# Kernel tuning notes

Measured on AMD Instinct MI355X. Metric: run time of the kernel, lower is better.

The kernel has to match this reference:

```python
import jax, jax.numpy as jnp
import numpy as np

B, N, D_MODEL = 4, 4096, 1024
HEADS, DIM_HEAD = 8, 64
INNER = HEADS * DIM_HEAD  # 512
NB_FEAT = int(DIM_HEAD * np.log(DIM_HEAD))  # 266, performer default
D_FF = 4 * D_MODEL
KERNEL_EPS = 1e-4
LN_EPS = 1e-5


def setup_inputs() -> dict:
    key = jax.random.key(0)
    ks = jax.random.split(key, 12)
    w = lambda i, shape: jax.random.normal(ks[i], shape, jnp.float32) * 0.02
    z = lambda *shape: jnp.zeros(shape, jnp.float32)
    o = lambda *shape: jnp.ones(shape, jnp.float32)
    return dict(
        x=jax.random.normal(ks[0], (B, N, D_MODEL), jnp.float32),
        proj_w=w(1, (D_MODEL, D_MODEL)), proj_b=z(D_MODEL),
        ln1_g=o(D_MODEL), ln1_b=z(D_MODEL),
        wq=w(2, (D_MODEL, INNER)), bq=z(INNER),
        wk=w(3, (D_MODEL, INNER)), bk=z(INNER),
        wv=w(4, (D_MODEL, INNER)), bv=z(INNER),
        wo=w(5, (INNER, D_MODEL)), bo=z(D_MODEL),
        proj_mat=jax.random.normal(ks[6], (NB_FEAT, DIM_HEAD), jnp.float32),
        ln2_g=o(D_MODEL), ln2_b=z(D_MODEL),
        w1=w(7, (D_MODEL, D_FF)), b1=z(D_FF),
        w2=w(8, (D_FF, D_MODEL)), b2=z(D_MODEL),
    )


def _layer_norm(x, g, b):
    mu = x.mean(-1, keepdims=True)
    var = ((x - mu) ** 2).mean(-1, keepdims=True)
    return (x - mu) * jax.lax.rsqrt(var + LN_EPS) * g + b


def _softmax_kernel(data, proj_mat, is_query):
    # data: [b,h,n,d], proj_mat: [m,d] -> features [b,h,n,m]
    dn = DIM_HEAD ** -0.25            # data_normalizer
    ratio = NB_FEAT ** -0.5
    dd = jnp.einsum('bhnd,md->bhnm', data * dn, proj_mat)
    diag = (data ** 2).sum(-1, keepdims=True) * (0.5 * dn * dn)
    if is_query:
        mx = dd.max(-1, keepdims=True)
    else:
        mx = dd.max(axis=(-1, -2), keepdims=True)
    return ratio * (jnp.exp(dd - diag - mx) + KERNEL_EPS)


def _favor_attention(q, k, v, proj_mat):
    # non-causal FAVOR+ linear attention; q,k,v: [b,h,n,d]
    qp = _softmax_kernel(q, proj_mat, True)    # [b,h,n,m]
    kp = _softmax_kernel(k, proj_mat, False)   # [b,h,n,m]
    k_sum = kp.sum(-2)                         # [b,h,m]
    d_inv = 1.0 / jnp.einsum('bhnm,bhm->bhn', qp, k_sum)
    ctx = jnp.einsum('bhnm,bhnd->bhmd', kp, v)
    return jnp.einsum('bhmd,bhnm,bhn->bhnd', ctx, qp, d_inv)


def _performer(x, ln1_g, ln1_b, wq, bq, wk, bk, wv, bv, wo, bo, proj_mat,
               ln2_g, ln2_b, w1, b1, w2, b2):
    # pre-norm self-attention block
    h = _layer_norm(x, ln1_g, ln1_b)
    split = lambda t: t.reshape(B, N, HEADS, DIM_HEAD).transpose(0, 2, 1, 3)
    q = split(h @ wq + bq)
    k = split(h @ wk + bk)
    v = split(h @ wv + bv)
    attn = _favor_attention(q, k, v, proj_mat)
    attn = attn.transpose(0, 2, 1, 3).reshape(B, N, INNER)
    x = x + attn @ wo + bo
    # pre-norm feed-forward block
    h = _layer_norm(x, ln2_g, ln2_b)
    x = x + jax.nn.gelu(h @ w1 + b1, approximate=False) @ w2 + b2
    return x


def reference(x, proj_w, proj_b, ln1_g, ln1_b, wq, bq, wk, bk, wv, bv,
              wo, bo, proj_mat, ln2_g, ln2_b, w1, b1, w2, b2):
    u = x @ proj_w + proj_b                    # dense gate branch
    v = _performer(x, ln1_g, ln1_b, wq, bq, wk, bk, wv, bv, wo, bo,
                   proj_mat, ln2_g, ln2_b, w1, b1, w2, b2)
    return u * v
```

## Files before the change

### kernel.cpp

```cpp
#include <hip/hip_runtime.h>
#include <math.h>

typedef unsigned short bf16_t;
using bf16x8 = __attribute__((ext_vector_type(8))) short;
using f32x4  = __attribute__((ext_vector_type(4))) float;

#define DEVFN static __device__ __forceinline__

DEVFN float b2f(bf16_t u){ unsigned v=((unsigned)u)<<16; float f; __builtin_memcpy(&f,&v,4); return f; }
DEVFN bf16_t f2b(float f){ unsigned u; __builtin_memcpy(&u,&f,4); u += 0x7fffu + ((u>>16)&1u); return (bf16_t)(u>>16); }
DEVFN unsigned encf(float f){ unsigned u=__float_as_uint(f); return (u&0x80000000u)? ~u : (u|0x80000000u); }
DEVFN float decf(unsigned e){ return __uint_as_float((e&0x80000000u)? (e^0x80000000u) : ~e); }

DEVFN float erf_fast(float x){
  float ax = fabsf(x);
  float t = __builtin_amdgcn_rcpf(1.0f + 0.3275911f*ax);
  float y = t*(0.254829592f + t*(-0.284496736f + t*(1.421413741f
          + t*(-1.453152027f + t*1.061405429f))));
  float r = 1.0f - y*__expf(-ax*ax);
  return copysignf(r, x);
}

constexpr float DN_SCALE = 0.35355339059327373f;
constexpr float RATIO    = 0.06131393394849658f;
constexpr float KEPS     = 1e-4f;
#define MPAD 288

#define GLOAD_LDS16(g, l) __builtin_amdgcn_global_load_lds( \
    (__attribute__((address_space(1))) void*)(g), \
    (__attribute__((address_space(3))) void*)(l), 16, 0, 0)

#define MFMA16(a,b,c) __builtin_amdgcn_mfma_f32_16x16x32_bf16(a,b,c,0,0,0)

__global__ __launch_bounds__(256)
void wt_cast(const float* __restrict__ W, bf16_t* __restrict__ Wt, int K, int N)
{
  __shared__ alignas(16) float ts[32][33];
  int t = threadIdx.x;
  int r = t>>3, c4 = (t&7)*4;
  int k0 = blockIdx.x*32, n0 = blockIdx.y*32;
  float4 v = *(const float4*)(W + (size_t)(k0+r)*N + n0 + c4);
  ts[r][c4+0]=v.x; ts[r][c4+1]=v.y; ts[r][c4+2]=v.z; ts[r][c4+3]=v.w;
  __syncthreads();
  ushort4 o;
  o.x = f2b(ts[c4+0][r]); o.y = f2b(ts[c4+1][r]);
  o.z = f2b(ts[c4+2][r]); o.w = f2b(ts[c4+3][r]);
  *(ushort4*)(Wt + (size_t)(n0+r)*K + k0 + c4) = o;
}

__global__ __launch_bounds__(256)
void concat_bias(const float* __restrict__ bq, const float* __restrict__ bk,
                 const float* __restrict__ bv, float* __restrict__ dst)
{
  int t = blockIdx.x*256 + threadIdx.x;
  if (t < 512) dst[t] = bq[t];
  else if (t < 1024) dst[t] = bk[t-512];
  else dst[t] = bv[t-1024];
}

__global__ void mx_init(unsigned* m){ if (threadIdx.x < 32) m[threadIdx.x] = 0u; }

__global__ void zero_out(float* o, long n){
  long i = (long)blockIdx.x*256 + threadIdx.x;
  if (i < n) o[i] = 0.f;
}

__global__ __launch_bounds__(256)
void pm_cast(const float* __restrict__ pm, bf16_t* __restrict__ pmb)
{
  int idx = blockIdx.x*256 + threadIdx.x;
  int r = idx>>6, c = idx&63;
  pmb[idx] = (r < 266) ? f2b(pm[r*64+c]*DN_SCALE) : (bf16_t)0;
}

__global__ __launch_bounds__(256)
void diag_kernel(const bf16_t* __restrict__ qkv, float* __restrict__ diagq,
                 float* __restrict__ diagk)
{
  int bh = blockIdx.y, b = bh>>3, h = bh&7;
  int n = blockIdx.x*256 + threadIdx.x;
  long trow = (long)b*4096 + n;
  const bf16_t* qp_ = qkv + trow*1536 + h*64;
  const bf16_t* kp_ = qkv + trow*1536 + 512 + h*64;
  float sq = 0.f, sk = 0.f;
  #pragma unroll
  for (int i=0;i<8;i++){
    uint4 cq = ((const uint4*)qp_)[i];
    uint4 ck = ((const uint4*)kp_)[i];
    unsigned w[4] = {cq.x,cq.y,cq.z,cq.w};
    unsigned v[4] = {ck.x,ck.y,ck.z,ck.w};
    #pragma unroll
    for (int j=0;j<4;j++){
      float a0=b2f((bf16_t)(w[j]&0xffff)), a1=b2f((bf16_t)(w[j]>>16));
      float b0=b2f((bf16_t)(v[j]&0xffff)), b1=b2f((bf16_t)(v[j]>>16));
      sq += a0*a0 + a1*a1; sk += b0*b0 + b1*b1;
    }
  }
  float sc = 0.5f*DN_SCALE*DN_SCALE;
  diagq[(long)bh*4096 + n] = sq*sc;
  diagk[(long)bh*4096 + n] = sk*sc;
}

__global__ __launch_bounds__(256)
void vt_trans(const bf16_t* __restrict__ qkv, bf16_t* __restrict__ vT)
{
  __shared__ ushort ts[32][36];
  int by = blockIdx.y;
  int bh = by>>1, dt = by&1, b = bh>>3, h = bh&7;
  int n0 = blockIdx.x*32;
  int t = threadIdx.x, r = t>>3, c4 = (t&7)*4;
  ushort4 v = *(const ushort4*)(qkv + ((size_t)b*4096 + n0 + r)*1536 + 1024 + h*64 + dt*32 + c4);
  ts[r][c4+0]=v.x; ts[r][c4+1]=v.y; ts[r][c4+2]=v.z; ts[r][c4+3]=v.w;
  __syncthreads();
  ushort4 o;
  o.x = ts[c4+0][r]; o.y = ts[c4+1][r]; o.z = ts[c4+2][r]; o.w = ts[c4+3][r];
  *(ushort4*)(vT + ((size_t)bh*64 + dt*32 + r)*4096 + n0 + c4) = o;
}

__global__ __launch_bounds__(256)
void ln_kernel(const float* __restrict__ x, const float* __restrict__ g,
               const float* __restrict__ b, bf16_t* __restrict__ out)
{
  long row = blockIdx.x; int t = threadIdx.x;
  float4 v = ((const float4*)x)[row*256 + t];
  float s = v.x+v.y+v.z+v.w;
  #pragma unroll
  for (int o=32;o>0;o>>=1) s += __shfl_xor(s, o);
  __shared__ float r1[4], r2[4];
  if ((t&63)==0) r1[t>>6] = s;
  __syncthreads();
  float mu = (r1[0]+r1[1]+r1[2]+r1[3]) * (1.f/1024.f);
  float dx = v.x-mu, dy = v.y-mu, dz = v.z-mu, dw = v.w-mu;
  float ss = dx*dx+dy*dy+dz*dz+dw*dw;
  #pragma unroll
  for (int o=32;o>0;o>>=1) ss += __shfl_xor(ss, o);
  if ((t&63)==0) r2[t>>6] = ss;
  __syncthreads();
  float var = (r2[0]+r2[1]+r2[2]+r2[3]) * (1.f/1024.f);
  float rs = rsqrtf(var + 1e-5f);
  float4 gg = ((const float4*)g)[t], bb = ((const float4*)b)[t];
  ushort4 o4;
  o4.x = f2b(dx*rs*gg.x+bb.x); o4.y = f2b(dy*rs*gg.y+bb.y);
  o4.z = f2b(dz*rs*gg.z+bb.z); o4.w = f2b(dw*rs*gg.w+bb.w);
  ((ushort4*)out)[row*256+t] = o4;
}

__global__ __launch_bounds__(256)
void cast_f32_bf16(const float* __restrict__ in, bf16_t* __restrict__ out)
{
  long i = (long)blockIdx.x*256 + threadIdx.x;
  float4 v = ((const float4*)in)[i];
  ushort4 o;
  o.x = f2b(v.x); o.y = f2b(v.y); o.z = f2b(v.z); o.w = f2b(v.w);
  ((ushort4*)out)[i] = o;
}

template<int RES, int GELU, int GATEF, int OBF>
__global__ __launch_bounds__(256)
void gemm_bt(const bf16_t* __restrict__ A, int lda,
             const bf16_t* __restrict__ Bt, int ldb,
             const float* __restrict__ bias,
             const float* res,
             const float* gatef,
             void* Cout, int N, int K)
{
  __shared__ alignas(16) bf16_t As[2][128*32];
  __shared__ alignas(16) bf16_t Bs[2][128*32];
  const int tid = threadIdx.x;
  const int wid = tid>>6, lane = tid&63;
  const int l15 = lane&15, l4 = lane>>4;
  const int wm = wid>>1, wn = wid&1;

  const int NX = gridDim.x;
  const int nwg = NX * gridDim.y;
  const int lid = blockIdx.y*NX + blockIdx.x;
  const int qc = nwg>>3;
  const int wgid = (lid&7)*qc + (lid>>3);
  const int stripe = wgid / (16*NX);
  const int rem    = wgid % (16*NX);
  const long m0 = (long)(stripe*16 + (rem & 15))*128;
  const long n0 = (long)(rem >> 4)*128;

  f32x4 acc[4][4];
  #pragma unroll
  for (int i=0;i<4;i++)
    #pragma unroll
    for (int j=0;j<4;j++) acc[i][j] = f32x4{0.f,0.f,0.f,0.f};

  const bf16_t* ga = A  + (size_t)(m0 + (tid>>2))*lda + (tid&3)*8;
  const bf16_t* gb = Bt + (size_t)(n0 + (tid>>2))*ldb + (tid&3)*8;

  auto STAGE = [&](int buf){
    GLOAD_LDS16(ga,                   &As[buf][wid*512]);
    GLOAD_LDS16(ga + (size_t)64*lda,  &As[buf][2048 + wid*512]);
    GLOAD_LDS16(gb,                   &Bs[buf][wid*512]);
    GLOAD_LDS16(gb + (size_t)64*ldb,  &Bs[buf][2048 + wid*512]);
    ga += 32; gb += 32;
  };

  const int nt = K >> 5;
  STAGE(0);
  __syncthreads();
  int cur = 0;
  for (int t = 0; t < nt; ++t){
    if (t+1 < nt) STAGE(cur^1);
    bf16x8 af[4], bfr[4];
    #pragma unroll
    for (int i=0;i<4;i++){
      af[i]  = *(const bf16x8*)(&As[cur][(wm*64 + i*16 + l15)*32 + l4*8]);
      bfr[i] = *(const bf16x8*)(&Bs[cur][(wn*64 + i*16 + l15)*32 + l4*8]);
    }
    #pragma unroll
    for (int i=0;i<4;i++)
      #pragma unroll
      for (int j=0;j<4;j++)
        acc[i][j] = MFMA16(af[i], bfr[j], acc[i][j]);
    __syncthreads();
    cur ^= 1;
  }

  #pragma unroll
  for (int i=0;i<4;i++){
    #pragma unroll
    for (int j=0;j<4;j++){
      #pragma unroll
      for (int r=0;r<4;r++){
        long row = m0 + wm*64 + i*16 + l4*4 + r;
        long col = n0 + wn*64 + j*16 + l15;
        float v = acc[i][j][r] + bias[col];
        if constexpr (RES)   v += res[row*(long)N + col];
        if constexpr (GELU)  v = 0.5f*v*(1.0f + erf_fast(v*0.70710678118654752f));
        if constexpr (GATEF) v *= gatef[row*(long)N + col];
        if constexpr (OBF)  ((bf16_t*)Cout)[row*(long)N + col] = f2b(v);
        else                ((float* )Cout)[row*(long)N + col] = v;
      }
    }
  }
}


__global__ __launch_bounds__(256,2)
void favor_kmax2(const bf16_t* __restrict__ qkv, const bf16_t* __restrict__ pmb,
                 unsigned* __restrict__ mxk)
{
  int bh = blockIdx.y, b = bh>>3, h = bh&7;
  int t = threadIdx.x, wid = t>>6, lane = t&63;
  int l15 = lane&15, l4 = lane>>4;
  int n0 = blockIdx.x*64, row0 = wid*16;
  f32x4 acc[18];
  #pragma unroll
  for (int c=0;c<18;c++) acc[c] = f32x4{0.f,0.f,0.f,0.f};
  const bf16_t* abase = qkv + ((size_t)(b*4096) + n0 + row0 + l15)*1536 + 512 + h*64;
  #pragma unroll
  for (int kh=0;kh<2;kh++){
    bf16x8 a = *(const bf16x8*)(abase + kh*32 + l4*8);
    #pragma unroll
    for (int ct=0;ct<18;ct++){
      bf16x8 bb = *(const bf16x8*)(pmb + (ct*16+l15)*64 + kh*32 + l4*8);
      acc[ct] = MFMA16(a, bb, acc[ct]);
    }
  }
  float mx = -3e38f;
  #pragma unroll
  for (int ct=0;ct<18;ct++){
    if (ct*16 + l15 < 266){
      #pragma unroll
      for (int r=0;r<4;r++) mx = fmaxf(mx, acc[ct][r]);
    }
  }
  #pragma unroll
  for (int o=32;o>0;o>>=1) mx = fmaxf(mx, __shfl_xor(mx, o));
  __shared__ float red[4];
  if (lane==0) red[wid] = mx;
  __syncthreads();
  if (t==0){
    float m2 = fmaxf(fmaxf(red[0],red[1]),fmaxf(red[2],red[3]));
    atomicMax(mxk + bh, encf(m2));
  }
}

__global__ __launch_bounds__(256,2)
void favor_kp(const bf16_t* __restrict__ qkv, const bf16_t* __restrict__ pmb,
              const unsigned* __restrict__ mxk, const float* __restrict__ diagk,
              bf16_t* __restrict__ kp, int bh0)
{
  int bhl = blockIdx.y, bh = bh0 + bhl, b = bh>>3, h = bh&7;
  int t = threadIdx.x, wid = t>>6, lane = t&63;
  int l15 = lane&15, l4 = lane>>4;
  int n0 = blockIdx.x*64, row0 = wid*16;
  f32x4 acc[18];
  #pragma unroll
  for (int c=0;c<18;c++) acc[c] = f32x4{0.f,0.f,0.f,0.f};
  const bf16_t* abase = qkv + ((size_t)(b*4096) + n0 + row0 + l15)*1536 + 512 + h*64;
  #pragma unroll
  for (int kh=0;kh<2;kh++){
    bf16x8 a = *(const bf16x8*)(abase + kh*32 + l4*8);
    #pragma unroll
    for (int ct=0;ct<18;ct++){
      bf16x8 bb = *(const bf16x8*)(pmb + (ct*16+l15)*64 + kh*32 + l4*8);
      acc[ct] = MFMA16(a, bb, acc[ct]);
    }
  }
  float MX = decf(mxk[bh]);
  float dg[4];
  #pragma unroll
  for (int r=0;r<4;r++) dg[r] = diagk[(size_t)bh*4096 + n0 + row0 + l4*4 + r];
  #pragma unroll
  for (int ct=0;ct<18;ct++){
    int col = ct*16 + l15;
    #pragma unroll
    for (int r=0;r<4;r++){
      float v = (col < 266) ? RATIO*(__expf(acc[ct][r] - dg[r] - MX) + KEPS) : 0.f;
      kp[((size_t)bhl*4096 + n0 + row0 + l4*4 + r)*MPAD + col] = f2b(v);
    }
  }
}

__global__ __launch_bounds__(256)
void trans_kp(const bf16_t* __restrict__ kp, bf16_t* __restrict__ kpT)
{
  __shared__ ushort ts[32][36];
  int bhl = blockIdx.z;
  int n0 = blockIdx.x*32, m0 = blockIdx.y*32;
  int t = threadIdx.x, r = t>>3, c4 = (t&7)*4;
  ushort4 v = *(const ushort4*)(kp + ((size_t)bhl*4096 + n0 + r)*MPAD + m0 + c4);
  ts[r][c4+0]=v.x; ts[r][c4+1]=v.y; ts[r][c4+2]=v.z; ts[r][c4+3]=v.w;
  __syncthreads();
  ushort4 o;
  o.x = ts[c4+0][r]; o.y = ts[c4+1][r]; o.z = ts[c4+2][r]; o.w = ts[c4+3][r];
  *(ushort4*)(kpT + ((size_t)bhl*MPAD + m0 + r)*4096 + n0 + c4) = o;
}

__global__ __launch_bounds__(256)
void ksum_kernel(const bf16_t* __restrict__ kpT, float* __restrict__ ksumf, int bh0)
{
  int t = threadIdx.x, wid = t>>6, lane = t&63;
  int rr = blockIdx.x*4 + wid;
  int bhl = rr/272, m = rr%272;
  const bf16_t* row = kpT + ((size_t)bhl*MPAD + m)*4096;
  float s = 0.f;
  #pragma unroll
  for (int j=0;j<8;j++){
    bf16x8 v = *(const bf16x8*)(row + j*512 + lane*8);
    #pragma unroll
    for (int e=0;e<8;e++) s += b2f((bf16_t)v[e]);
  }
  #pragma unroll
  for (int o=32;o>0;o>>=1) s += __shfl_xor(s, o);
  if (lane==0) ksumf[(size_t)(bh0+bhl)*MPAD + m] = s;
}

__global__ __launch_bounds__(256,2)
void ctx_gemm(const bf16_t* __restrict__ kpT, const bf16_t* __restrict__ vT,
              float* __restrict__ ctxP, int bh0)
{
  int m0 = blockIdx.x*16, ks = blockIdx.y, bhl = blockIdx.z, bh = bh0 + bhl;
  int t = threadIdx.x, wid = t>>6, lane = t&63;
  int l15 = lane&15, l4 = lane>>4;
  f32x4 acc[4];
  #pragma unroll
  for (int c=0;c<4;c++) acc[c] = f32x4{0.f,0.f,0.f,0.f};
  const bf16_t* Abase = kpT + ((size_t)bhl*MPAD + m0 + l15)*4096;
  const bf16_t* Bbase = vT + ((size_t)bh*64)*4096;
  const int kb = ks*1024 + wid*256;
  for (int k = kb; k < kb + 256; k += 32){
    bf16x8 a = *(const bf16x8*)(Abase + k + l4*8);
    #pragma unroll
    for (int ct=0;ct<4;ct++){
      bf16x8 bb = *(const bf16x8*)(Bbase + (size_t)(ct*16+l15)*4096 + k + l4*8);
      acc[ct] = MFMA16(a, bb, acc[ct]);
    }
  }
  __shared__ float red[4][4][16][16];
  #pragma unroll
  for (int ct=0;ct<4;ct++)
    #pragma unroll
    for (int r=0;r<4;r++) red[wid][ct][l4*4+r][l15] = acc[ct][r];
  __syncthreads();
  #pragma unroll
  for (int i=0;i<4;i++){
    int e = i*256 + t;
    int ct = e>>8, row = (e>>4)&15, col = e&15;
    float s = ((red[0][ct][row][col] + red[1][ct][row][col])
             + (red[2][ct][row][col] + red[3][ct][row][col]));
    ctxP[(((size_t)bhl*4 + ks)*272 + m0 + row)*64 + ct*16 + col] = s;
  }
}

__global__ __launch_bounds__(256)
void ctx_reduce(const float* __restrict__ ctxP, bf16_t* __restrict__ ctxT, int bh0)
{
  int bhl = blockIdx.y, bh = bh0 + bhl;
  int idx = blockIdx.x*256 + threadIdx.x;
  int m = idx>>6, d = idx&63;
  float s = 0.f;
  #pragma unroll
  for (int ks=0;ks<4;ks++)
    s += ctxP[(((size_t)bhl*4 + ks)*272 + m)*64 + d];
  ctxT[((size_t)bh*64 + d)*MPAD + m] = f2b(s);
}

__global__ __launch_bounds__(256,2)
void favor_q(const bf16_t* __restrict__ qkv, const bf16_t* __restrict__ pmb,
             const float* __restrict__ diagq, const float* __restrict__ ksumf,
             const bf16_t* __restrict__ ctxT, bf16_t* __restrict__ attn)
{
  __shared__ alignas(16) ushort qpLds[64*296];
  __shared__ float ksLds[288];
  int bh = blockIdx.y, b = bh>>3, h = bh&7;
  int t = threadIdx.x, wid = t>>6, lane = t&63;
  int l15 = lane&15, l4 = lane>>4;
  int n0 = blockIdx.x*64, row0 = wid*16;
  ksLds[t] = ksumf[(size_t)bh*MPAD + t];
  if (t < 32) ksLds[256+t] = ksumf[(size_t)bh*MPAD + 256 + t];
  __syncthreads();

  f32x4 acc[18];
  #pragma unroll
  for (int c=0;c<18;c++) acc[c] = f32x4{0.f,0.f,0.f,0.f};
  const bf16_t* abase = qkv + ((size_t)(b*4096) + n0 + row0 + l15)*1536 + h*64;
  #pragma unroll
  for (int kh=0;kh<2;kh++){
    bf16x8 a = *(const bf16x8*)(abase + kh*32 + l4*8);
    #pragma unroll
    for (int ct=0;ct<18;ct++){
      bf16x8 bb = *(const bf16x8*)(pmb + (ct*16+l15)*64 + kh*32 + l4*8);
      acc[ct] = MFMA16(a, bb, acc[ct]);
    }
  }
  float mxr[4] = {-3e38f,-3e38f,-3e38f,-3e38f};
  #pragma unroll
  for (int ct=0;ct<18;ct++){
    if (ct*16 + l15 < 266){
      #pragma unroll
      for (int r=0;r<4;r++) mxr[r] = fmaxf(mxr[r], acc[ct][r]);
    }
  }
  #pragma unroll
  for (int r=0;r<4;r++){
    mxr[r] = fmaxf(mxr[r], __shfl_xor(mxr[r], 1));
    mxr[r] = fmaxf(mxr[r], __shfl_xor(mxr[r], 2));
    mxr[r] = fmaxf(mxr[r], __shfl_xor(mxr[r], 4));
    mxr[r] = fmaxf(mxr[r], __shfl_xor(mxr[r], 8));
  }
  float dg[4];
  #pragma unroll
  for (int r=0;r<4;r++) dg[r] = diagq[(size_t)bh*4096 + n0 + row0 + l4*4 + r];
  float den[4] = {0.f,0.f,0.f,0.f};
  #pragma unroll
  for (int ct=0;ct<18;ct++){
    int col = ct*16 + l15;
    float ks = ksLds[col];
    #pragma unroll
    for (int r=0;r<4;r++){
      float qpv = 0.f;
      if (col < 266){
        qpv = RATIO*(__expf(acc[ct][r] - dg[r] - mxr[r]) + KEPS);
        den[r] += qpv*ks;
      }
      qpLds[(row0 + l4*4 + r)*296 + col] = f2b(qpv);
    }
  }
  float dinv[4];
  #pragma unroll
  for (int r=0;r<4;r++){
    den[r] += __shfl_xor(den[r], 1);
    den[r] += __shfl_xor(den[r], 2);
    den[r] += __shfl_xor(den[r], 4);
    den[r] += __shfl_xor(den[r], 8);
    dinv[r] = 1.0f/den[r];
  }
  __syncthreads();

  f32x4 o2[4];
  #pragma unroll
  for (int c=0;c<4;c++) o2[c] = f32x4{0.f,0.f,0.f,0.f};
  const bf16_t* Bbase = ctxT + (size_t)bh*64*MPAD;
  #pragma unroll
  for (int kk=0;kk<9;kk++){
    int k0 = kk*32;
    bf16x8 a = *(const bf16x8*)&qpLds[(row0 + l15)*296 + k0 + l4*8];
    #pragma unroll
    for (int ct=0;ct<4;ct++){
      bf16x8 bb = *(const bf16x8*)(Bbase + (size_t)(ct*16+l15)*MPAD + k0 + l4*8);
      o2[ct] = MFMA16(a, bb, o2[ct]);
    }
  }
  #pragma unroll
  for (int ct=0;ct<4;ct++)
    #pragma unroll
    for (int r=0;r<4;r++)
      attn[((size_t)(b*4096) + n0 + row0 + l4*4 + r)*512 + h*64 + ct*16 + l15]
        = f2b(o2[ct][r] * dinv[r]);
}

extern "C" void kernel_launch(void* const* d_in, const int* in_sizes, int n_in,
                              void* d_out, int out_size, void* d_ws, size_t ws_size,
                              hipStream_t stream)
{
  (void)in_sizes; (void)n_in; (void)out_size;
  const float* x      = (const float*)d_in[0];
  const float* proj_w = (const float*)d_in[1];
  const float* proj_b = (const float*)d_in[2];
  const float* ln1_g  = (const float*)d_in[3];
  const float* ln1_b  = (const float*)d_in[4];
  const float* wq     = (const float*)d_in[5];
  const float* bq     = (const float*)d_in[6];
  const float* wk     = (const float*)d_in[7];
  const float* bk     = (const float*)d_in[8];
  const float* wv     = (const float*)d_in[9];
  const float* bv     = (const float*)d_in[10];
  const float* wo     = (const float*)d_in[11];
  const float* bo     = (const float*)d_in[12];
  const float* pm     = (const float*)d_in[13];
  const float* ln2_g  = (const float*)d_in[14];
  const float* ln2_b  = (const float*)d_in[15];
  const float* w1     = (const float*)d_in[16];
  const float* b1     = (const float*)d_in[17];
  const float* w2     = (const float*)d_in[18];
  const float* b2     = (const float*)d_in[19];
  float* out = (float*)d_out;
  const size_t MB = 1ull<<20;

  char* ws = (char*)d_ws;
  size_t off = 0;
  auto alloc = [&](size_t bytes)->void*{ void* p = ws + off; off += (bytes + 255) & ~(size_t)255; return p; };
  bf16_t* Wt_proj = (bf16_t*)alloc(2ul*1024*1024);
  bf16_t* Wt_qkv  = (bf16_t*)alloc(2ul*1536*1024);
  bf16_t* Wt_o    = (bf16_t*)alloc(2ul*1024*512);
  bf16_t* Wt_1    = (bf16_t*)alloc(2ul*4096*1024);
  bf16_t* Wt_2    = (bf16_t*)alloc(2ul*1024*4096);
  float*  bqkv    = (float*) alloc(4ul*1536);
  unsigned* mxk   = (unsigned*)alloc(4ul*32);
  bf16_t* pmb     = (bf16_t*)alloc(2ul*MPAD*64);
  float*  diagq   = (float*) alloc(4ul*32*4096);
  float*  diagk   = (float*) alloc(4ul*32*4096);
  float*  ksumf   = (float*) alloc(4ul*32*MPAD);
  bf16_t* ctxT    = (bf16_t*)alloc(2ul*32*64*MPAD);
  float*  ctxP    = (float*) alloc(4ul*8*4*272*64);
  char*   R       = (char*)  alloc(0);
  size_t R_avail = (ws_size > off) ? ws_size - off : 0;

  if (R_avail < 67*MB){ zero_out<<<dim3(65536), 256, 0, stream>>>(out, 16777216L); return; }
  int KG = (R_avail >= 87*MB) ? 8 : 4;
  int NC = (R_avail >= 84*MB) ? 2 : 4;

  bf16_t* qkv  = (bf16_t*)(R);
  bf16_t* h1c  = (bf16_t*)(R + 48*MB);
  bf16_t* kp   = (bf16_t*)(R + 48*MB);
  bf16_t* kpT  = (bf16_t*)(R + 48*MB + (size_t)KG*4096*MPAD*2 + 1*MB);
  bf16_t* attn = (bf16_t*)(R + 48*MB);
  long    CH   = 16384/NC;
  bf16_t* h2c  = (bf16_t*)(R);
  bf16_t* ff1c = (bf16_t*)(R + 16*MB);
  bf16_t* vT   = (bf16_t*)d_out;

  wt_cast<<<dim3(32,32), 256, 0, stream>>>(proj_w, Wt_proj, 1024, 1024);
  wt_cast<<<dim3(32,16), 256, 0, stream>>>(wq, Wt_qkv,              1024, 512);
  wt_cast<<<dim3(32,16), 256, 0, stream>>>(wk, Wt_qkv + 512*1024,   1024, 512);
  wt_cast<<<dim3(32,16), 256, 0, stream>>>(wv, Wt_qkv + 1024*1024,  1024, 512);
  wt_cast<<<dim3(16,32), 256, 0, stream>>>(wo, Wt_o, 512, 1024);
  wt_cast<<<dim3(32,128),256, 0, stream>>>(w1, Wt_1, 1024, 4096);
  wt_cast<<<dim3(128,32),256, 0, stream>>>(w2, Wt_2, 4096, 1024);
  concat_bias<<<dim3(6), 256, 0, stream>>>(bq, bk, bv, bqkv);
  pm_cast<<<dim3(72), 256, 0, stream>>>(pm, pmb);

  for (int c = 0; c < 2; c++){
    ln_kernel<<<dim3(8192), 256, 0, stream>>>(x + (size_t)c*8192*1024, ln1_g, ln1_b, h1c);
    gemm_bt<0,0,0,1><<<dim3(12,64), 256, 0, stream>>>(h1c, 1024, Wt_qkv, 1024,
        bqkv, nullptr, nullptr, qkv + (size_t)c*8192*1536, 1536, 1024);
  }

  diag_kernel<<<dim3(16,32), 256, 0, stream>>>(qkv, diagq, diagk);
  vt_trans<<<dim3(128,64), 256, 0, stream>>>(qkv, vT);
  mx_init<<<dim3(1), 64, 0, stream>>>(mxk);
  favor_kmax2<<<dim3(64,32), 256, 0, stream>>>(qkv, pmb, mxk);
  for (int g = 0; g < 32; g += KG){
    favor_kp<<<dim3(64,KG), 256, 0, stream>>>(qkv, pmb, mxk, diagk, kp, g);
    trans_kp<<<dim3(128,9,KG), 256, 0, stream>>>(kp, kpT);
    ksum_kernel<<<dim3(KG*68), 256, 0, stream>>>(kpT, ksumf, g);
    ctx_gemm<<<dim3(17,4,KG), 256, 0, stream>>>(kpT, vT, ctxP, g);
    ctx_reduce<<<dim3(68,KG), 256, 0, stream>>>(ctxP, ctxT, g);
  }
  favor_q<<<dim3(64,32), 256, 0, stream>>>(qkv, pmb, diagq, ksumf, ctxT, attn);

  gemm_bt<1,0,0,0><<<dim3(8,128), 256, 0, stream>>>(attn, 512, Wt_o, 512,
      bo, x, nullptr, out, 1024, 512);

  for (int c = 0; c < NC; c++){
    float* xrow = out + (size_t)c*CH*1024;
    ln_kernel<<<dim3((unsigned)CH), 256, 0, stream>>>(xrow, ln2_g, ln2_b, h2c);
    gemm_bt<0,1,0,1><<<dim3(32,(unsigned)(CH/128)), 256, 0, stream>>>(h2c, 1024, Wt_1, 1024,
        b1, nullptr, nullptr, ff1c, 4096, 1024);
    gemm_bt<1,0,0,0><<<dim3(8,(unsigned)(CH/128)), 256, 0, stream>>>(ff1c, 4096, Wt_2, 4096,
        b2, xrow, nullptr, xrow, 1024, 4096);
    cast_f32_bf16<<<dim3((unsigned)CH), 256, 0, stream>>>(x + (size_t)c*CH*1024, h2c);
    gemm_bt<0,0,1,0><<<dim3(8,(unsigned)(CH/128)), 256, 0, stream>>>(h2c, 1024, Wt_proj, 1024,
        proj_b, nullptr, xrow, xrow, 1024, 1024);
  }
}
```

Baseline: 994.4 us.

## Triple-buffer GEMM LDS pipeline and fuse diag and kp transpose into FAVOR kernels

The GEMM main loop moves from a double-buffered LDS pipeline to three stages. It issues loads two tiles ahead and uses explicit vmcnt waits with hard barriers, so global latency is better hidden. Separately, the row squared-norm (diag) is now computed inside favor_kp and favor_q from the MFMA operand registers, which removes diag_kernel and its buffers. favor_kp also writes kp transposed directly, which removes the trans_kp pass. ctx_reduce is extended to zero-fill the padded rows; the extra LDS and strided transposed stores are the trade-offs.

```diff
diff --git a/kernel.cpp b/kernel.cpp
--- a/kernel.cpp
+++ b/kernel.cpp
@@ -32,6 +32,13 @@
 
 #define MFMA16(a,b,c) __builtin_amdgcn_mfma_f32_16x16x32_bf16(a,b,c,0,0,0)
 
+DEVFN void hard_barrier(){
+  __builtin_amdgcn_sched_barrier(0);
+  asm volatile("s_barrier" ::: "memory");
+  __builtin_amdgcn_sched_barrier(0);
+}
+#define WAITVM(N) asm volatile("s_waitcnt vmcnt(" #N ")" ::: "memory")
+
 __global__ __launch_bounds__(256)
 void wt_cast(const float* __restrict__ W, bf16_t* __restrict__ Wt, int K, int N)
 {
@@ -71,34 +78,6 @@
   int idx = blockIdx.x*256 + threadIdx.x;
   int r = idx>>6, c = idx&63;
   pmb[idx] = (r < 266) ? f2b(pm[r*64+c]*DN_SCALE) : (bf16_t)0;
-}
-
-__global__ __launch_bounds__(256)
-void diag_kernel(const bf16_t* __restrict__ qkv, float* __restrict__ diagq,
-                 float* __restrict__ diagk)
-{
-  int bh = blockIdx.y, b = bh>>3, h = bh&7;
-  int n = blockIdx.x*256 + threadIdx.x;
-  long trow = (long)b*4096 + n;
-  const bf16_t* qp_ = qkv + trow*1536 + h*64;
-  const bf16_t* kp_ = qkv + trow*1536 + 512 + h*64;
-  float sq = 0.f, sk = 0.f;
-  #pragma unroll
-  for (int i=0;i<8;i++){
-    uint4 cq = ((const uint4*)qp_)[i];
-    uint4 ck = ((const uint4*)kp_)[i];
-    unsigned w[4] = {cq.x,cq.y,cq.z,cq.w};
-    unsigned v[4] = {ck.x,ck.y,ck.z,ck.w};
-    #pragma unroll
-    for (int j=0;j<4;j++){
-      float a0=b2f((bf16_t)(w[j]&0xffff)), a1=b2f((bf16_t)(w[j]>>16));
-      float b0=b2f((bf16_t)(v[j]&0xffff)), b1=b2f((bf16_t)(v[j]>>16));
-      sq += a0*a0 + a1*a1; sk += b0*b0 + b1*b1;
-    }
-  }
-  float sc = 0.5f*DN_SCALE*DN_SCALE;
-  diagq[(long)bh*4096 + n] = sq*sc;
-  diagk[(long)bh*4096 + n] = sk*sc;
 }
 
 __global__ __launch_bounds__(256)
@@ -164,8 +143,8 @@
              const float* gatef,
              void* Cout, int N, int K)
 {
-  __shared__ alignas(16) bf16_t As[2][128*32];
-  __shared__ alignas(16) bf16_t Bs[2][128*32];
+  __shared__ alignas(16) bf16_t As[3][128*32];
+  __shared__ alignas(16) bf16_t Bs[3][128*32];
   const int tid = threadIdx.x;
   const int wid = tid>>6, lane = tid&63;
   const int l15 = lane&15, l4 = lane>>4;
@@ -190,33 +169,38 @@
   const bf16_t* ga = A  + (size_t)(m0 + (tid>>2))*lda + (tid&3)*8;
   const bf16_t* gb = Bt + (size_t)(n0 + (tid>>2))*ldb + (tid&3)*8;
 
-  auto STAGE = [&](int buf){
-    GLOAD_LDS16(ga,                   &As[buf][wid*512]);
-    GLOAD_LDS16(ga + (size_t)64*lda,  &As[buf][2048 + wid*512]);
-    GLOAD_LDS16(gb,                   &Bs[buf][wid*512]);
-    GLOAD_LDS16(gb + (size_t)64*ldb,  &Bs[buf][2048 + wid*512]);
+  auto STAGE = [&](bf16_t* Ab, bf16_t* Bb){
+    GLOAD_LDS16(ga,                   Ab + wid*512);
+    GLOAD_LDS16(ga + (size_t)64*lda,  Ab + 2048 + wid*512);
+    GLOAD_LDS16(gb,                   Bb + wid*512);
+    GLOAD_LDS16(gb + (size_t)64*ldb,  Bb + 2048 + wid*512);
     ga += 32; gb += 32;
   };
 
   const int nt = K >> 5;
-  STAGE(0);
-  __syncthreads();
-  int cur = 0;
+  STAGE(As[0], Bs[0]);
+  STAGE(As[1], Bs[1]);
+  int i0 = 0, i1 = 1, i2 = 2;
   for (int t = 0; t < nt; ++t){
-    if (t+1 < nt) STAGE(cur^1);
+    if (t+2 < nt){ STAGE(As[i2], Bs[i2]); WAITVM(8); }
+    else if (t+1 < nt){ WAITVM(4); }
+    else { WAITVM(0); }
+    hard_barrier();
+    const bf16_t* Ab = As[i0];
+    const bf16_t* Bb = Bs[i0];
     bf16x8 af[4], bfr[4];
     #pragma unroll
     for (int i=0;i<4;i++){
-      af[i]  = *(const bf16x8*)(&As[cur][(wm*64 + i*16 + l15)*32 + l4*8]);
-      bfr[i] = *(const bf16x8*)(&Bs[cur][(wn*64 + i*16 + l15)*32 + l4*8]);
+      af[i]  = *(const bf16x8*)(Ab + (wm*64 + i*16 + l15)*32 + l4*8);
+      bfr[i] = *(const bf16x8*)(Bb + (wn*64 + i*16 + l15)*32 + l4*8);
     }
     #pragma unroll
     for (int i=0;i<4;i++)
       #pragma unroll
       for (int j=0;j<4;j++)
         acc[i][j] = MFMA16(af[i], bfr[j], acc[i][j]);
-    __syncthreads();
-    cur ^= 1;
+    hard_barrier();
+    int tmp = i0; i0 = i1; i1 = i2; i2 = tmp;
   }
 
   #pragma unroll
@@ -281,8 +265,7 @@
 
 __global__ __launch_bounds__(256,2)
 void favor_kp(const bf16_t* __restrict__ qkv, const bf16_t* __restrict__ pmb,
-              const unsigned* __restrict__ mxk, const float* __restrict__ diagk,
-              bf16_t* __restrict__ kp, int bh0)
+              const unsigned* __restrict__ mxk, bf16_t* __restrict__ kpT, int bh0)
 {
   int bhl = blockIdx.y, bh = bh0 + bhl, b = bh>>3, h = bh&7;
   int t = threadIdx.x, wid = t>>6, lane = t&63;
@@ -292,43 +275,37 @@
   #pragma unroll
   for (int c=0;c<18;c++) acc[c] = f32x4{0.f,0.f,0.f,0.f};
   const bf16_t* abase = qkv + ((size_t)(b*4096) + n0 + row0 + l15)*1536 + 512 + h*64;
+  float rsq = 0.f;
   #pragma unroll
   for (int kh=0;kh<2;kh++){
     bf16x8 a = *(const bf16x8*)(abase + kh*32 + l4*8);
+    #pragma unroll
+    for (int e=0;e<8;e++){ float v = b2f((bf16_t)a[e]); rsq += v*v; }
     #pragma unroll
     for (int ct=0;ct<18;ct++){
       bf16x8 bb = *(const bf16x8*)(pmb + (ct*16+l15)*64 + kh*32 + l4*8);
       acc[ct] = MFMA16(a, bb, acc[ct]);
     }
   }
+  rsq += __shfl_xor(rsq, 16);
+  rsq += __shfl_xor(rsq, 32);
   float MX = decf(mxk[bh]);
+  constexpr float DSC = 0.5f*DN_SCALE*DN_SCALE;
   float dg[4];
   #pragma unroll
-  for (int r=0;r<4;r++) dg[r] = diagk[(size_t)bh*4096 + n0 + row0 + l4*4 + r];
+  for (int r=0;r<4;r++) dg[r] = DSC * __shfl(rsq, l4*4 + r);
   #pragma unroll
   for (int ct=0;ct<18;ct++){
     int col = ct*16 + l15;
-    #pragma unroll
-    for (int r=0;r<4;r++){
-      float v = (col < 266) ? RATIO*(__expf(acc[ct][r] - dg[r] - MX) + KEPS) : 0.f;
-      kp[((size_t)bhl*4096 + n0 + row0 + l4*4 + r)*MPAD + col] = f2b(v);
-    }
-  }
-}
-
-__global__ __launch_bounds__(256)
-void trans_kp(const bf16_t* __restrict__ kp, bf16_t* __restrict__ kpT)
-{
-  __shared__ ushort ts[32][36];
-  int bhl = blockIdx.z;
-  int n0 = blockIdx.x*32, m0 = blockIdx.y*32;
-  int t = threadIdx.x, r = t>>3, c4 = (t&7)*4;
-  ushort4 v = *(const ushort4*)(kp + ((size_t)bhl*4096 + n0 + r)*MPAD + m0 + c4);
-  ts[r][c4+0]=v.x; ts[r][c4+1]=v.y; ts[r][c4+2]=v.z; ts[r][c4+3]=v.w;
-  __syncthreads();
-  ushort4 o;
-  o.x = ts[c4+0][r]; o.y = ts[c4+1][r]; o.z = ts[c4+2][r]; o.w = ts[c4+3][r];
-  *(ushort4*)(kpT + ((size_t)bhl*MPAD + m0 + r)*4096 + n0 + c4) = o;
+    ushort4 o;
+    if (col < 266){
+      o.x = f2b(RATIO*(__expf(acc[ct][0] - dg[0] - MX) + KEPS));
+      o.y = f2b(RATIO*(__expf(acc[ct][1] - dg[1] - MX) + KEPS));
+      o.z = f2b(RATIO*(__expf(acc[ct][2] - dg[2] - MX) + KEPS));
+      o.w = f2b(RATIO*(__expf(acc[ct][3] - dg[3] - MX) + KEPS));
+    } else { o.x=0; o.y=0; o.z=0; o.w=0; }
+    *(ushort4*)(kpT + ((size_t)bhl*MPAD + col)*4096 + n0 + row0 + l4*4) = o;
+  }
 }
 
 __global__ __launch_bounds__(256)
@@ -394,15 +371,17 @@
   int idx = blockIdx.x*256 + threadIdx.x;
   int m = idx>>6, d = idx&63;
   float s = 0.f;
-  #pragma unroll
-  for (int ks=0;ks<4;ks++)
-    s += ctxP[(((size_t)bhl*4 + ks)*272 + m)*64 + d];
+  if (m < 272){
+    #pragma unroll
+    for (int ks=0;ks<4;ks++)
+      s += ctxP[(((size_t)bhl*4 + ks)*272 + m)*64 + d];
+  }
   ctxT[((size_t)bh*64 + d)*MPAD + m] = f2b(s);
 }
 
 __global__ __launch_bounds__(256,2)
 void favor_q(const bf16_t* __restrict__ qkv, const bf16_t* __restrict__ pmb,
-             const float* __restrict__ diagq, const float* __restrict__ ksumf,
+             const float* __restrict__ ksumf,
              const bf16_t* __restrict__ ctxT, bf16_t* __restrict__ attn)
 {
   __shared__ alignas(16) ushort qpLds[64*296];
@@ -419,15 +398,25 @@
   #pragma unroll
   for (int c=0;c<18;c++) acc[c] = f32x4{0.f,0.f,0.f,0.f};
   const bf16_t* abase = qkv + ((size_t)(b*4096) + n0 + row0 + l15)*1536 + h*64;
+  float rsq = 0.f;
   #pragma unroll
   for (int kh=0;kh<2;kh++){
     bf16x8 a = *(const bf16x8*)(abase + kh*32 + l4*8);
+    #pragma unroll
+    for (int e=0;e<8;e++){ float v = b2f((bf16_t)a[e]); rsq += v*v; }
     #pragma unroll
     for (int ct=0;ct<18;ct++){
       bf16x8 bb = *(const bf16x8*)(pmb + (ct*16+l15)*64 + kh*32 + l4*8);
       acc[ct] = MFMA16(a, bb, acc[ct]);
     }
   }
+  rsq += __shfl_xor(rsq, 16);
+  rsq += __shfl_xor(rsq, 32);
+  constexpr float DSC = 0.5f*DN_SCALE*DN_SCALE;
+  float dg[4];
+  #pragma unroll
+  for (int r=0;r<4;r++) dg[r] = DSC * __shfl(rsq, l4*4 + r);
+
   float mxr[4] = {-3e38f,-3e38f,-3e38f,-3e38f};
   #pragma unroll
   for (int ct=0;ct<18;ct++){
@@ -443,9 +432,6 @@
     mxr[r] = fmaxf(mxr[r], __shfl_xor(mxr[r], 4));
     mxr[r] = fmaxf(mxr[r], __shfl_xor(mxr[r], 8));
   }
-  float dg[4];
-  #pragma unroll
-  for (int r=0;r<4;r++) dg[r] = diagq[(size_t)bh*4096 + n0 + row0 + l4*4 + r];
   float den[4] = {0.f,0.f,0.f,0.f};
   #pragma unroll
   for (int ct=0;ct<18;ct++){
@@ -533,8 +519,6 @@
   float*  bqkv    = (float*) alloc(4ul*1536);
   unsigned* mxk   = (unsigned*)alloc(4ul*32);
   bf16_t* pmb     = (bf16_t*)alloc(2ul*MPAD*64);
-  float*  diagq   = (float*) alloc(4ul*32*4096);
-  float*  diagk   = (float*) alloc(4ul*32*4096);
   float*  ksumf   = (float*) alloc(4ul*32*MPAD);
   bf16_t* ctxT    = (bf16_t*)alloc(2ul*32*64*MPAD);
   float*  ctxP    = (float*) alloc(4ul*8*4*272*64);
@@ -547,8 +531,7 @@
 
   bf16_t* qkv  = (bf16_t*)(R);
   bf16_t* h1c  = (bf16_t*)(R + 48*MB);
-  bf16_t* kp   = (bf16_t*)(R + 48*MB);
-  bf16_t* kpT  = (bf16_t*)(R + 48*MB + (size_t)KG*4096*MPAD*2 + 1*MB);
+  bf16_t* kpT  = (bf16_t*)(R + 48*MB);
   bf16_t* attn = (bf16_t*)(R + 48*MB);
   long    CH   = 16384/NC;
   bf16_t* h2c  = (bf16_t*)(R);
@@ -571,18 +554,16 @@
         bqkv, nullptr, nullptr, qkv + (size_t)c*8192*1536, 1536, 1024);
   }
 
-  diag_kernel<<<dim3(16,32), 256, 0, stream>>>(qkv, diagq, diagk);
   vt_trans<<<dim3(128,64), 256, 0, stream>>>(qkv, vT);
   mx_init<<<dim3(1), 64, 0, stream>>>(mxk);
   favor_kmax2<<<dim3(64,32), 256, 0, stream>>>(qkv, pmb, mxk);
   for (int g = 0; g < 32; g += KG){
-    favor_kp<<<dim3(64,KG), 256, 0, stream>>>(qkv, pmb, mxk, diagk, kp, g);
-    trans_kp<<<dim3(128,9,KG), 256, 0, stream>>>(kp, kpT);
+    favor_kp<<<dim3(64,KG), 256, 0, stream>>>(qkv, pmb, mxk, kpT, g);
     ksum_kernel<<<dim3(KG*68), 256, 0, stream>>>(kpT, ksumf, g);
     ctx_gemm<<<dim3(17,4,KG), 256, 0, stream>>>(kpT, vT, ctxP, g);
-    ctx_reduce<<<dim3(68,KG), 256, 0, stream>>>(ctxP, ctxT, g);
-  }
-  favor_q<<<dim3(64,32), 256, 0, stream>>>(qkv, pmb, diagq, ksumf, ctxT, attn);
+    ctx_reduce<<<dim3(72,KG), 256, 0, stream>>>(ctxP, ctxT, g);
+  }
+  favor_q<<<dim3(64,32), 256, 0, stream>>>(qkv, pmb, ksumf, ctxT, attn);
 
   gemm_bt<1,0,0,0><<<dim3(8,128), 256, 0, stream>>>(attn, 512, Wt_o, 512,
       bo, x, nullptr, out, 1024, 512);
```

Result: slower. 1.032 ms (+3.7%).
